# Optimization experiments

Hardware: AMD Instinct MI355X
Metric: run time of the kernel (lower is better)

The kernel has to match this reference:

```python
import jax, jax.numpy as jnp
import numpy as np

MIN_SIZE = 16.0 / 800.0
PRE_NMS_TOP_K = 6000   # mode='test'
POST_NMS_TOP_K = 300   # mode='test'
IOU_THR = 0.7
H = W = 100
A = 9
N = H * W * A


def setup_inputs() -> dict:
    key = jax.random.key(0)
    k1, k2, k3 = jax.random.split(key, 3)
    pred_cls = jax.random.normal(k1, (1, H, W, 2 * A), dtype=jnp.float32)
    pred_reg = jax.random.normal(k2, (1, N, 4), dtype=jnp.float32) * 0.2
    # anchors as valid normalized xyxy boxes
    u = jax.random.uniform(k3, (N, 4), dtype=jnp.float32)
    cx = 0.05 + 0.9 * u[:, 0]
    cy = 0.05 + 0.9 * u[:, 1]
    w = 0.02 + 0.18 * u[:, 2]
    h = 0.02 + 0.18 * u[:, 3]
    anchor = jnp.stack([cx - w / 2, cy - h / 2, cx + w / 2, cy + h / 2], axis=1)
    return {"pred_cls": pred_cls, "pred_reg": pred_reg, "anchor": anchor}


def greedy_nms_mask(boxes, valid):
    # boxes: [K,4] sorted by descending score; valid: [K] bool
    K = boxes.shape[0]
    area = (boxes[:, 2] - boxes[:, 0]) * (boxes[:, 3] - boxes[:, 1])
    lt = jnp.maximum(boxes[:, None, :2], boxes[None, :, :2])   # [K,K,2]
    rb = jnp.minimum(boxes[:, None, 2:], boxes[None, :, 2:])
    wh = jnp.clip(rb - lt, 0.0)
    inter = wh[..., 0] * wh[..., 1]
    union = area[:, None] + area[None, :] - inter
    iou = inter / jnp.maximum(union, jnp.float32(1e-12))       # [K,K]
    idx = jnp.arange(K)

    def body(i, suppressed):
        keep_i = jnp.logical_not(suppressed[i]) & valid[i]
        return suppressed | (keep_i & (iou[i] > IOU_THR) & (idx > i))

    suppressed = jax.lax.fori_loop(0, K, body, jnp.zeros((K,), dtype=bool))
    return jnp.logical_not(suppressed) & valid


def reference(pred_cls, pred_reg, anchor):
    reg = pred_reg.reshape(-1, 4)                 # squeeze -> [N,4]
    # xy_to_cxcy(anchor)
    a_cxcy = jnp.concatenate([(anchor[:, 2:] + anchor[:, :2]) / 2,
                              anchor[:, 2:] - anchor[:, :2]], axis=1)
    # decode(reg, anchor_cxcy)
    cxcy = reg[:, :2] * a_cxcy[:, 2:] + a_cxcy[:, :2]
    wh = jnp.exp(reg[:, 2:]) * a_cxcy[:, 2:]
    # cxcy_to_xy(...).clamp(0,1)
    roi = jnp.clip(jnp.concatenate([cxcy - wh / 2, cxcy + wh / 2], axis=1), 0.0, 1.0)

    # objectness softmax over the 2-class logits
    probs = jax.nn.softmax(pred_cls.reshape(1, H, W, A, 2), axis=-1)[..., 1].reshape(-1)  # [N]

    # size filter
    ws = roi[:, 2] - roi[:, 0]
    hs = roi[:, 3] - roi[:, 1]
    size_ok = (hs >= MIN_SIZE) & (ws >= MIN_SIZE)
    masked_scores = jnp.where(size_ok, probs, -jnp.inf)

    # sort descending + take pre-NMS top-k (filtered boxes sort last)
    top_scores, top_idx = jax.lax.top_k(masked_scores, PRE_NMS_TOP_K)
    boxes = roi[top_idx]                           # [K,4]
    valid = size_ok[top_idx]

    kept = greedy_nms_mask(boxes, valid)           # [K] bool

    # first POST_NMS_TOP_K kept boxes in score order; pad with zeros
    rank = jnp.cumsum(kept.astype(jnp.int32)) - 1
    slot = jnp.where(kept & (rank < POST_NMS_TOP_K), rank, POST_NMS_TOP_K)
    out = jnp.zeros((POST_NMS_TOP_K, 4), dtype=boxes.dtype).at[slot].set(boxes, mode='drop')
    return out
```

## Files before the change

kernel.cpp:

```cpp
#include <hip/hip_runtime.h>
#include <stdint.h>

#pragma clang fp contract(off)

#define N_ANCH 90000
#define M_TOP  1024
#define M_L    512
#define NW_L   8
#define K_POST 300
#define CAP    2048
#define WINB   0x3D00
#define WINSZ  768
#define DB     32
#define MIN_SIZE (16.0f / 800.0f)
#define IOU_THR  0.7f

#define SIDX(j) ((j) + ((j) >> 6))
#define SB_SZ   (M_L + NW_L)

#define OFF_HISTB 0
#define OFF_CNT   98304
#define OFF_CAND  98368
#define OFF_ROI   114752
#define OFF_KEYS  1554752
#define OFF_SBOX  1914752
#define OFF_MASK  1931136

__global__ void __launch_bounds__(1024)
decode_score_kernel(const float2* __restrict__ cls,
                    const float4* __restrict__ reg,
                    const float4* __restrict__ anc,
                    float4* __restrict__ roi,
                    unsigned* __restrict__ keys,
                    int* __restrict__ histB) {
    __shared__ int lh[WINSZ];
    int tid = threadIdx.x;
    for (int k = tid; k < WINSZ; k += 1024) lh[k] = 0;
    __syncthreads();

    for (int n = blockIdx.x * 1024 + tid; n < N_ANCH; n += DB * 1024) {
        float4 a = anc[n];
        float4 r = reg[n];
        float aw  = a.z - a.x;
        float ah  = a.w - a.y;
        float acx = (a.z + a.x) * 0.5f;
        float acy = (a.w + a.y) * 0.5f;
        float cx = r.x * aw + acx;
        float cy = r.y * ah + acy;
        float w  = expf(r.z) * aw;
        float h  = expf(r.w) * ah;
        float x1 = fminf(fmaxf(cx - w * 0.5f, 0.0f), 1.0f);
        float y1 = fminf(fmaxf(cy - h * 0.5f, 0.0f), 1.0f);
        float x2 = fminf(fmaxf(cx + w * 0.5f, 0.0f), 1.0f);
        float y2 = fminf(fmaxf(cy + h * 0.5f, 0.0f), 1.0f);
        roi[n] = make_float4(x1, y1, x2, y2);

        float2 c = cls[n];
        float m  = fmaxf(c.x, c.y);
        float e0 = expf(c.x - m);
        float e1 = expf(c.y - m);
        float p  = e1 / (e0 + e1);

        bool ok = ((x2 - x1) >= MIN_SIZE) && ((y2 - y1) >= MIN_SIZE);
        unsigned key = ok ? (__float_as_uint(p) ^ 0x80000000u) : 0u;
        keys[n] = key;
        if (key != 0u) {
            int hb = (int)(key >> 16) - 0x8000;
            if (hb >= WINB) atomicAdd(&lh[hb - WINB], 1);
        }
    }
    __syncthreads();
    for (int k = tid; k < WINSZ; k += 1024)
        histB[blockIdx.x * WINSZ + k] = lh[k];
}

__global__ void __launch_bounds__(1024)
thrcompact_kernel(const unsigned* __restrict__ keys,
                  const int* __restrict__ histB,
                  int* __restrict__ cnt,
                  unsigned long long* __restrict__ cand) {
    __shared__ int rscan[1024];
    __shared__ int s_pos;
    __shared__ unsigned s_thr;
    int t = threadIdx.x;
    if (t == 0) s_pos = 0;
    int wsum = 0;
    if (t < WINSZ) {
        int bin = WINSZ - 1 - t;
#pragma unroll
        for (int b = 0; b < DB; ++b) wsum += histB[b * WINSZ + bin];
    }
    rscan[t] = wsum;
    __syncthreads();
    for (int off = 1; off < 1024; off <<= 1) {
        int add = (t >= off) ? rscan[t - off] : 0;
        __syncthreads();
        rscan[t] += add;
        __syncthreads();
    }
    if (t < WINSZ && rscan[t] >= M_TOP && (t == 0 || rscan[t - 1] < M_TOP))
        s_thr = ((unsigned)(0x8000 + WINB + (WINSZ - 1 - t))) << 16;
    if (t == 0 && rscan[WINSZ - 1] < M_TOP)
        s_thr = 0x80000000u;
    __syncthreads();
    unsigned thr = s_thr;
    const uint4* k4 = (const uint4*)keys;
    for (int g = t; g < N_ANCH / 4; g += 1024) {
        uint4 kv = k4[g];
        int n0 = g * 4;
        if (kv.x >= thr) { int p = atomicAdd(&s_pos, 1); if (p < CAP) cand[p] = ((unsigned long long)kv.x << 32) | (unsigned)(~(unsigned)n0); }
        if (kv.y >= thr) { int p = atomicAdd(&s_pos, 1); if (p < CAP) cand[p] = ((unsigned long long)kv.y << 32) | (unsigned)(~(unsigned)(n0 + 1)); }
        if (kv.z >= thr) { int p = atomicAdd(&s_pos, 1); if (p < CAP) cand[p] = ((unsigned long long)kv.z << 32) | (unsigned)(~(unsigned)(n0 + 2)); }
        if (kv.w >= thr) { int p = atomicAdd(&s_pos, 1); if (p < CAP) cand[p] = ((unsigned long long)kv.w << 32) | (unsigned)(~(unsigned)(n0 + 3)); }
    }
    __syncthreads();
    if (t == 0) cnt[0] = (s_pos < CAP) ? s_pos : CAP;
}

__global__ void __launch_bounds__(1024)
rank_select_kernel(const unsigned long long* __restrict__ cand,
                   const int* __restrict__ cnt,
                   const float4* __restrict__ roi,
                   float4* __restrict__ sbox) {
    __shared__ unsigned long long s[CAP];
    __shared__ int red[1024];
    int tid = threadIdx.x;
    int c = cnt[0];
    if (c > CAP) c = CAP;
    for (int k = tid; k < CAP; k += 1024) s[k] = (k < c) ? cand[k] : 0ULL;
    __syncthreads();
    int e = tid & 63;
    int slice = tid >> 6;
    int i = blockIdx.x * 64 + e;
    unsigned long long v = (i < c) ? s[i] : 0ULL;
    int cnt_gt = 0;
    if (i < c) {
        int kbeg = slice * (CAP / 16);
        int kend = kbeg + (CAP / 16);
        if (kend > c) kend = c;
#pragma unroll 4
        for (int k = kbeg; k < kend; ++k)
            cnt_gt += (s[k] > v) ? 1 : 0;
    }
    red[tid] = cnt_gt;
    __syncthreads();
    if (slice == 0 && i < c) {
        int rank = 0;
#pragma unroll
        for (int q = 0; q < 16; ++q) rank += red[e + 64 * q];
        if (rank < M_TOP) {
            unsigned idx = ~((unsigned)v);
            sbox[rank] = roi[idx];
        }
    }
}

__global__ void __launch_bounds__(256)
mask_kernel(const float4* __restrict__ sbox,
            unsigned long long* __restrict__ mask) {
    __shared__ float4 sb[SB_SZ];
    int tid = threadIdx.x;
#pragma unroll
    for (int q = 0; q < M_L / 256; ++q) {
        int j = tid + q * 256;
        sb[SIDX(j)] = sbox[j];
    }
    __syncthreads();
    int wid = blockIdx.x * 256 + tid;
    int i = wid >> 3;
    int w = wid & 7;
    unsigned long long bits = 0;
    int j0 = w << 6;
    if (j0 + 63 > i) {
        float4 bi = sb[SIDX(i)];
        float ai = (bi.z - bi.x) * (bi.w - bi.y);
        for (int b = 0; b < 64; ++b) {
            int j = j0 + b;
            if (j > i) {
                float4 bj = sb[SIDX(j)];
                float xx1 = fmaxf(bi.x, bj.x);
                float yy1 = fmaxf(bi.y, bj.y);
                float xx2 = fminf(bi.z, bj.z);
                float yy2 = fminf(bi.w, bj.w);
                float ww = fmaxf(xx2 - xx1, 0.0f);
                float hh = fmaxf(yy2 - yy1, 0.0f);
                float inter = ww * hh;
                float aj = (bj.z - bj.x) * (bj.w - bj.y);
                float uni = ai + aj - inter;
                float iou = inter / fmaxf(uni, 1e-12f);
                if (iou > IOU_THR) bits |= 1ull << b;
            }
        }
    }
    mask[wid] = bits;
}

__device__ __forceinline__ unsigned long long readlane64(unsigned long long v, int sl) {
    unsigned lo = (unsigned)__builtin_amdgcn_readlane((int)(unsigned)v, sl);
    unsigned hi = (unsigned)__builtin_amdgcn_readlane((int)(unsigned)(v >> 32), sl);
    return ((unsigned long long)hi << 32) | lo;
}

__global__ void __launch_bounds__(64)
walk_kernel(const unsigned long long* __restrict__ mask,
            const float4* __restrict__ sbox,
            const int* __restrict__ cnt,
            float4* __restrict__ out) {
    __shared__ int s_keep[K_POST];
    __shared__ int s_kc;
    int lane = threadIdx.x;
    int c_eff = cnt[0];
    if (c_eff > M_TOP) c_eff = M_TOP;

    unsigned long long diag[NW_L];
#pragma unroll
    for (int cc = 0; cc < NW_L; ++cc)
        diag[cc] = mask[(((cc << 6) | lane) << 3) + cc];

    unsigned long long remw = 0;
    int w = lane & 7;
    int kgrp = lane >> 3;
    int kc = 0;
    bool stop = false;
#pragma unroll
    for (int cc = 0; cc < NW_L; ++cc) {
        int base = cc << 6;
        unsigned long long valid =
            (c_eff >= base + 64) ? ~0ull
          : ((c_eff <= base) ? 0ull : ((1ull << (c_eff - base)) - 1ull));
        unsigned long long live = valid & ~readlane64(remw, cc);
        unsigned long long keptbits = 0;
        while (live) {
            int b = __ffsll((unsigned long long)live) - 1;
            keptbits |= 1ull << b;
            if (lane == 0) s_keep[kc] = base + b;
            ++kc;
            if (kc >= K_POST) { stop = true; break; }
            live &= ~readlane64(diag[cc], b);
            live &= ~(1ull << b);
        }
        if (stop) break;
        if (cc == NW_L - 1) break;
        if (keptbits) {
            int nk = __popcll(keptbits);
            int mypos = 0;
            if (lane < nk) {
                unsigned long long tmp = keptbits;
                for (int p = 0; p < lane; ++p) tmp &= tmp - 1;
                mypos = base + (__ffsll((unsigned long long)tmp) - 1);
            }
            unsigned long long acc = 0;
#pragma unroll
            for (int r = 0; r < 8; ++r) {
                int kg = (r << 3) | kgrp;
                int row = __shfl(mypos, kg);
                unsigned long long v = (kg < nk) ? mask[(row << 3) + w] : 0ull;
                acc |= v;
            }
            acc |= __shfl_xor(acc, 8);
            acc |= __shfl_xor(acc, 16);
            acc |= __shfl_xor(acc, 32);
            remw |= acc;
        }
    }
    if (!stop) {
        for (int i = M_L; i < c_eff && kc < K_POST; ++i) {
            float4 bi = sbox[i];
            float ai = (bi.z - bi.x) * (bi.w - bi.y);
            bool any = false;
            for (int k = lane; k < kc; k += 64) {
                float4 bk = sbox[s_keep[k]];
                float xx1 = fmaxf(bi.x, bk.x);
                float yy1 = fmaxf(bi.y, bk.y);
                float xx2 = fminf(bi.z, bk.z);
                float yy2 = fminf(bi.w, bk.w);
                float ww = fmaxf(xx2 - xx1, 0.0f);
                float hh = fmaxf(yy2 - yy1, 0.0f);
                float inter = ww * hh;
                float ak = (bk.z - bk.x) * (bk.w - bk.y);
                float uni = ai + ak - inter;
                if (inter / fmaxf(uni, 1e-12f) > IOU_THR) any = true;
            }
            if (__ballot(any) == 0ull) {
                if (lane == 0) s_keep[kc] = i;
                ++kc;
            }
        }
    }
    if (lane == 0) s_kc = kc;
    __syncthreads();
    int kcf = s_kc;
    for (int j = lane; j < K_POST; j += 64)
        out[j] = (j < kcf) ? sbox[s_keep[j]] : make_float4(0.f, 0.f, 0.f, 0.f);
}

extern "C" void kernel_launch(void* const* d_in, const int* in_sizes, int n_in,
                              void* d_out, int out_size, void* d_ws, size_t ws_size,
                              hipStream_t stream) {
    const float2* cls = (const float2*)d_in[0];
    const float4* reg = (const float4*)d_in[1];
    const float4* anc = (const float4*)d_in[2];
    float4* out = (float4*)d_out;

    char* ws = (char*)d_ws;
    int*       histB = (int*)(ws + OFF_HISTB);
    int*       cnt   = (int*)(ws + OFF_CNT);
    unsigned long long* cand = (unsigned long long*)(ws + OFF_CAND);
    float4*    roi   = (float4*)(ws + OFF_ROI);
    unsigned*  keys  = (unsigned*)(ws + OFF_KEYS);
    float4*    sbox  = (float4*)(ws + OFF_SBOX);
    unsigned long long* mask = (unsigned long long*)(ws + OFF_MASK);

    decode_score_kernel<<<DB, 1024, 0, stream>>>(cls, reg, anc, roi, keys, histB);
    thrcompact_kernel<<<1, 1024, 0, stream>>>(keys, histB, cnt, cand);
    rank_select_kernel<<<CAP / 64, 1024, 0, stream>>>(cand, cnt, roi, sbox);
    mask_kernel<<<M_L * NW_L / 256, 256, 0, stream>>>(sbox, mask);
    walk_kernel<<<1, 64, 0, stream>>>(mask, sbox, cnt, out);
}
```

Measured before the change: 136.1 us.

## Fuse threshold compaction and rank selection into one kernel, double decode blocks

```diff
diff --git a/kernel.cpp b/kernel.cpp
--- a/kernel.cpp
+++ b/kernel.cpp
@@ -11,7 +11,7 @@
 #define CAP    2048
 #define WINB   0x3D00
 #define WINSZ  768
-#define DB     32
+#define DB     64
 #define MIN_SIZE (16.0f / 800.0f)
 #define IOU_THR  0.7f
 
@@ -19,12 +19,11 @@
 #define SB_SZ   (M_L + NW_L)
 
 #define OFF_HISTB 0
-#define OFF_CNT   98304
-#define OFF_CAND  98368
-#define OFF_ROI   114752
-#define OFF_KEYS  1554752
-#define OFF_SBOX  1914752
-#define OFF_MASK  1931136
+#define OFF_CNT   196608
+#define OFF_ROI   196672
+#define OFF_KEYS  1636672
+#define OFF_SBOX  1996672
+#define OFF_MASK  2013056
 
 __global__ void __launch_bounds__(1024)
 decode_score_kernel(const float2* __restrict__ cls,
@@ -75,11 +74,13 @@
 }
 
 __global__ void __launch_bounds__(1024)
-thrcompact_kernel(const unsigned* __restrict__ keys,
-                  const int* __restrict__ histB,
-                  int* __restrict__ cnt,
-                  unsigned long long* __restrict__ cand) {
+select_kernel(const unsigned* __restrict__ keys,
+              const int* __restrict__ histB,
+              const float4* __restrict__ roi,
+              int* __restrict__ cnt,
+              float4* __restrict__ sbox) {
     __shared__ int rscan[1024];
+    __shared__ unsigned long long scand[CAP];
     __shared__ int s_pos;
     __shared__ unsigned s_thr;
     int t = threadIdx.x;
@@ -87,7 +88,6 @@
     int wsum = 0;
     if (t < WINSZ) {
         int bin = WINSZ - 1 - t;
-#pragma unroll
         for (int b = 0; b < DB; ++b) wsum += histB[b * WINSZ + bin];
     }
     rscan[t] = wsum;
@@ -108,46 +108,20 @@
     for (int g = t; g < N_ANCH / 4; g += 1024) {
         uint4 kv = k4[g];
         int n0 = g * 4;
-        if (kv.x >= thr) { int p = atomicAdd(&s_pos, 1); if (p < CAP) cand[p] = ((unsigned long long)kv.x << 32) | (unsigned)(~(unsigned)n0); }
-        if (kv.y >= thr) { int p = atomicAdd(&s_pos, 1); if (p < CAP) cand[p] = ((unsigned long long)kv.y << 32) | (unsigned)(~(unsigned)(n0 + 1)); }
-        if (kv.z >= thr) { int p = atomicAdd(&s_pos, 1); if (p < CAP) cand[p] = ((unsigned long long)kv.z << 32) | (unsigned)(~(unsigned)(n0 + 2)); }
-        if (kv.w >= thr) { int p = atomicAdd(&s_pos, 1); if (p < CAP) cand[p] = ((unsigned long long)kv.w << 32) | (unsigned)(~(unsigned)(n0 + 3)); }
-    }
-    __syncthreads();
-    if (t == 0) cnt[0] = (s_pos < CAP) ? s_pos : CAP;
-}
-
-__global__ void __launch_bounds__(1024)
-rank_select_kernel(const unsigned long long* __restrict__ cand,
-                   const int* __restrict__ cnt,
-                   const float4* __restrict__ roi,
-                   float4* __restrict__ sbox) {
-    __shared__ unsigned long long s[CAP];
-    __shared__ int red[1024];
-    int tid = threadIdx.x;
-    int c = cnt[0];
+        if (kv.x >= thr) { int p = atomicAdd(&s_pos, 1); if (p < CAP) scand[p] = ((unsigned long long)kv.x << 32) | (unsigned)(~(unsigned)n0); }
+        if (kv.y >= thr) { int p = atomicAdd(&s_pos, 1); if (p < CAP) scand[p] = ((unsigned long long)kv.y << 32) | (unsigned)(~(unsigned)(n0 + 1)); }
+        if (kv.z >= thr) { int p = atomicAdd(&s_pos, 1); if (p < CAP) scand[p] = ((unsigned long long)kv.z << 32) | (unsigned)(~(unsigned)(n0 + 2)); }
+        if (kv.w >= thr) { int p = atomicAdd(&s_pos, 1); if (p < CAP) scand[p] = ((unsigned long long)kv.w << 32) | (unsigned)(~(unsigned)(n0 + 3)); }
+    }
+    __syncthreads();
+    int c = s_pos;
     if (c > CAP) c = CAP;
-    for (int k = tid; k < CAP; k += 1024) s[k] = (k < c) ? cand[k] : 0ULL;
-    __syncthreads();
-    int e = tid & 63;
-    int slice = tid >> 6;
-    int i = blockIdx.x * 64 + e;
-    unsigned long long v = (i < c) ? s[i] : 0ULL;
-    int cnt_gt = 0;
-    if (i < c) {
-        int kbeg = slice * (CAP / 16);
-        int kend = kbeg + (CAP / 16);
-        if (kend > c) kend = c;
-#pragma unroll 4
-        for (int k = kbeg; k < kend; ++k)
-            cnt_gt += (s[k] > v) ? 1 : 0;
-    }
-    red[tid] = cnt_gt;
-    __syncthreads();
-    if (slice == 0 && i < c) {
+    if (t == 0) cnt[0] = c;
+    for (int i = t; i < c; i += 1024) {
+        unsigned long long v = scand[i];
         int rank = 0;
-#pragma unroll
-        for (int q = 0; q < 16; ++q) rank += red[e + 64 * q];
+        for (int k = 0; k < c; ++k)
+            rank += (scand[k] > v) ? 1 : 0;
         if (rank < M_TOP) {
             unsigned idx = ~((unsigned)v);
             sbox[rank] = roi[idx];
@@ -305,15 +279,13 @@
     char* ws = (char*)d_ws;
     int*       histB = (int*)(ws + OFF_HISTB);
     int*       cnt   = (int*)(ws + OFF_CNT);
-    unsigned long long* cand = (unsigned long long*)(ws + OFF_CAND);
     float4*    roi   = (float4*)(ws + OFF_ROI);
     unsigned*  keys  = (unsigned*)(ws + OFF_KEYS);
     float4*    sbox  = (float4*)(ws + OFF_SBOX);
     unsigned long long* mask = (unsigned long long*)(ws + OFF_MASK);
 
     decode_score_kernel<<<DB, 1024, 0, stream>>>(cls, reg, anc, roi, keys, histB);
-    thrcompact_kernel<<<1, 1024, 0, stream>>>(keys, histB, cnt, cand);
-    rank_select_kernel<<<CAP / 64, 1024, 0, stream>>>(cand, cnt, roi, sbox);
+    select_kernel<<<1, 1024, 0, stream>>>(keys, histB, roi, cnt, sbox);
     mask_kernel<<<M_L * NW_L / 256, 256, 0, stream>>>(sbox, mask);
     walk_kernel<<<1, 64, 0, stream>>>(mask, sbox, cnt, out);
 }
```

New measurement: 163.6 us. 20.2% more time.
